# Kernel tuning notes

Measured on AMD Instinct MI355X. Metric: run time of the kernel, lower is better.

The kernel has to match this reference:

```python
import jax, jax.numpy as jnp
import numpy as np


def setup_inputs() -> dict:
    key = jax.random.key(0)
    ks = jax.random.split(key, 8)
    B, L, D = 4, 2048, 2048
    H, Dh, S = 24, 64, 64
    Di = H * Dh              # 1536
    P = H * (1 + 2 * S)      # 3096
    return {
        "hidden_states": jax.random.normal(ks[0], (B, L, D), jnp.float32),
        "norm_w": jnp.ones((D,), jnp.float32),
        "in_proj_w": jax.random.normal(ks[1], (2 * Di, D), jnp.float32) * 0.02,
        "in_proj_b": jnp.zeros((2 * Di,), jnp.float32),
        "conv_w": jax.random.normal(ks[2], (Di, 1, 4), jnp.float32) * 0.2,
        "conv_b": jnp.zeros((Di,), jnp.float32),
        "x_proj_w": jax.random.normal(ks[3], (P, Di), jnp.float32) * 0.02,
        "x_proj_b": jnp.zeros((P,), jnp.float32),
        "A_log": jnp.full((H,), np.log(0.5), jnp.float32),
        "log2_alpha_base": jnp.full((H,), -1.0, jnp.float32),
        "log2_beta": jnp.zeros((H,), jnp.float32),
        "surprise_ema": jnp.ones((H,), jnp.float32),
        "out_proj_w": jax.random.normal(ks[4], (D, Di), jnp.float32) * 0.02,
        "out_proj_b": jnp.zeros((D,), jnp.float32),
        "res_gate": jnp.full((1,), 1.0 / np.sqrt(2 * 24), jnp.float32),
    }


def reference(hidden_states, norm_w, in_proj_w, in_proj_b, conv_w, conv_b,
              x_proj_w, x_proj_b, A_log, log2_alpha_base, log2_beta,
              surprise_ema, out_proj_w, out_proj_b, res_gate):
    Bsz, L, D = hidden_states.shape
    H = A_log.shape[0]
    S = (x_proj_b.shape[0] // H - 1) // 2
    Di = in_proj_w.shape[0] // 2
    Dh = Di // H
    eps = jnp.finfo(jnp.float32).eps

    # RMSNorm
    x = hidden_states * jax.lax.rsqrt(jnp.mean(hidden_states ** 2, -1, keepdims=True) + eps) * norm_w
    # in_proj -> split x/z
    xz = x @ in_proj_w.T + in_proj_b
    x, z = xz[..., :Di], xz[..., Di:]
    # causal depthwise conv1d (kernel 4, left pad 3 == torch pad=3 then [:, :L])
    xc = jax.lax.conv_general_dilated(
        x.transpose(0, 2, 1), conv_w, (1,), [(3, 0)],
        dimension_numbers=("NCH", "OIH", "NCH"), feature_group_count=Di)
    x = jax.nn.silu((xc + conv_b[None, :, None]).transpose(0, 2, 1))
    # x_proj -> dt, B, C
    xp = (x @ x_proj_w.T + x_proj_b).reshape(Bsz, L, H, 1 + 2 * S)
    dt = xp[..., 0]
    Bs = xp[..., 1:1 + S]
    Cs = xp[..., 1 + S:]
    Bs = Bs / jnp.maximum(jnp.linalg.norm(Bs, axis=-1, keepdims=True), 1e-12)
    Cs = Cs / jnp.maximum(jnp.linalg.norm(Cs, axis=-1, keepdims=True), 1e-12)
    # dt-scaled log decay (dt_scale = softplus(dt))
    A = jnp.clip(A_log, -2.3, -0.01)[None, None, :] * jax.nn.softplus(dt)
    A_decay = jnp.exp(A)                       # [B, L, H]
    X = x.reshape(Bsz, L, H, Dh)

    # surprise-gate constants (eval mode: EMA buffer fixed)
    alpha_base = 1.0 - 2.0 ** jnp.clip(log2_alpha_base, -3.32, -0.015)   # [H]
    beta = 2.0 ** jnp.clip(log2_beta, -2.0, 2.0)                          # [H]

    def step(carry, xs):
        h, h_red = carry                      # [B,H,S,Dh], [B,H,S]
        x_t, a_t, B_t, C_t = xs               # [B,H,Dh], [B,H], [B,H,S], [B,H,S]
        u_red = B_t * x_t.mean(-1)[..., None]                 # mean over Dh of outer product
        diff = (1.0 - a_t)[..., None] * u_red                 # h_new_reduced - h_expected
        pe = jnp.mean(diff ** 2, -1)                          # [B,H]
        ns = pe / (surprise_ema[None, :] + 1e-6)
        boost = jax.nn.relu(jnp.tanh(beta[None, :] * ns))
        alpha = jnp.clip(alpha_base[None, :] + (1.0 - alpha_base[None, :]) * boost, 0.01, 0.999)
        u_t = B_t[..., None] * x_t[:, :, None, :]             # [B,H,S,Dh]
        h = alpha[..., None, None] * h + (1.0 - alpha)[..., None, None] * u_t
        h_red = h.mean(-1)
        y = jnp.einsum("bhs,bhsd->bhd", C_t, h)
        return (h, h_red), y

    h0 = jnp.zeros((Bsz, H, S, Dh), jnp.float32)
    hr0 = jnp.zeros((Bsz, H, S), jnp.float32)
    xs = (X.transpose(1, 0, 2, 3), A_decay.transpose(1, 0, 2),
          Bs.transpose(1, 0, 2, 3), Cs.transpose(1, 0, 2, 3))
    _, Yt = jax.lax.scan(step, (h0, hr0), xs)                 # [L,B,H,Dh]
    Y = Yt.transpose(1, 0, 2, 3).reshape(Bsz, L, Di)
    Y = Y * jax.nn.silu(z)
    out = Y @ out_proj_w.T + out_proj_b
    return hidden_states + res_gate * out
```

## Files before the change

### kernel.cpp

```cpp
#include <hip/hip_runtime.h>
#include <stdint.h>

#define BB 4
#define LLEN 2048
#define DMODEL 2048
#define NH 24
#define DH 64
#define SS 64
#define DI 1536
#define N2 3072
#define NP 3096
#define NP_PAD 3200
#define MROWS 8192
#define NCHUNK 16
#define QC 128

using bf16x8 = __bf16 __attribute__((ext_vector_type(8)));
using f32x4  = float __attribute__((ext_vector_type(4)));

__device__ __forceinline__ unsigned short f2bf(float f) {
  union { float f; unsigned int u; } v; v.f = f;
  unsigned int u = v.u + 0x7fffu + ((v.u >> 16) & 1u);
  return (unsigned short)(u >> 16);
}
__device__ __forceinline__ float bf2f(unsigned short h) {
  union { unsigned int u; float f; } v; v.u = ((unsigned int)h) << 16;
  return v.f;
}

__device__ __forceinline__ void gload16(const void* g, void* l) {
  __builtin_amdgcn_global_load_lds(
    reinterpret_cast<const __attribute__((address_space(1))) void*>(reinterpret_cast<uintptr_t>(g)),
    reinterpret_cast<__attribute__((address_space(3))) void*>((uint32_t)(reinterpret_cast<uintptr_t>(l))),
    16, 0, 0);
}

__global__ __launch_bounds__(256) void k_w2bf(const float* __restrict__ s,
                                              unsigned short* __restrict__ d,
                                              int n_src, int n_dst) {
  int i = blockIdx.x * 256 + threadIdx.x;
  if (i < n_dst) d[i] = (i < n_src) ? f2bf(s[i]) : (unsigned short)0;
}

__global__ __launch_bounds__(256) void k_rmsnorm(const float* __restrict__ hs,
                                                 const float* __restrict__ w,
                                                 unsigned short* __restrict__ out) {
  const int row = blockIdx.x;
  const int t = threadIdx.x;
  const float* x = hs + (size_t)row * DMODEL;
  float4 v0 = reinterpret_cast<const float4*>(x)[t * 2 + 0];
  float4 v1 = reinterpret_cast<const float4*>(x)[t * 2 + 1];
  float ss = v0.x * v0.x + v0.y * v0.y + v0.z * v0.z + v0.w * v0.w +
             v1.x * v1.x + v1.y * v1.y + v1.z * v1.z + v1.w * v1.w;
#pragma unroll
  for (int o = 32; o; o >>= 1) ss += __shfl_xor(ss, o);
  __shared__ float red[4];
  if ((t & 63) == 0) red[t >> 6] = ss;
  __syncthreads();
  ss = red[0] + red[1] + red[2] + red[3];
  const float r = rsqrtf(ss * (1.0f / DMODEL) + 1.1920928955078125e-07f);
  float4 w0 = reinterpret_cast<const float4*>(w)[t * 2 + 0];
  float4 w1 = reinterpret_cast<const float4*>(w)[t * 2 + 1];
  union { unsigned short u[8]; uint4 v; } pk;
  pk.u[0] = f2bf(v0.x * r * w0.x); pk.u[1] = f2bf(v0.y * r * w0.y);
  pk.u[2] = f2bf(v0.z * r * w0.z); pk.u[3] = f2bf(v0.w * r * w0.w);
  pk.u[4] = f2bf(v1.x * r * w1.x); pk.u[5] = f2bf(v1.y * r * w1.y);
  pk.u[6] = f2bf(v1.z * r * w1.z); pk.u[7] = f2bf(v1.w * r * w1.w);
  *reinterpret_cast<uint4*>(out + (size_t)row * DMODEL + t * 8) = pk.v;
}

template <int EPI, int BMH>
__global__ __launch_bounds__(512, 2)
void k_gemm5(const unsigned short* __restrict__ A, const unsigned short* __restrict__ B,
             const float* __restrict__ bias, void* __restrict__ Cv,
             const float* __restrict__ resid, const float* __restrict__ gatep,
             int K, int NT_N, int Nout, int ldc) {
  constexpr int NSET = BMH / 64;
  constexpr int AELEM = BMH * 64;
  constexpr int BUFE = AELEM + 16384;
  __shared__ alignas(16) unsigned short sm[2 * BUFE];
  const int tid = threadIdx.x;
  const int lane = tid & 63, wid = tid >> 6;
  const int wm = wid >> 2, wn = wid & 3;
  const int fr = lane & 15, kg = lane >> 4;
  const int nwg = gridDim.x;
  const int wg = ((int)blockIdx.x & 7) * (nwg >> 3) + ((int)blockIdx.x >> 3);
  const int m0 = (wg / NT_N) * BMH, n0 = (wg % NT_N) * 256;
  const int NT = K >> 6;

  const unsigned short* asrc[NSET];
  const unsigned short* bsrc[4];
#pragma unroll
  for (int li = 0; li < NSET; ++li) {
    const int gi = li * 512 + tid, r = gi >> 3, q = gi & 7;
    asrc[li] = A + (size_t)(m0 + r) * K + ((q ^ (r & 7)) << 3);
  }
#pragma unroll
  for (int li = 0; li < 4; ++li) {
    const int gi = li * 512 + tid, r = gi >> 3, q = gi & 7;
    bsrc[li] = B + (size_t)(n0 + r) * K + ((q ^ (r & 7)) << 3);
  }
  const int wlds = wid * 64;

#define STG5(buf, ko)                                                          \
  { unsigned short* da_ = sm + (buf) * BUFE;                                   \
    _Pragma("unroll") for (int li = 0; li < NSET; ++li)                        \
      gload16(asrc[li] + (ko), da_ + ((li * 512 + wlds) << 3));                \
    unsigned short* db_ = sm + (buf) * BUFE + AELEM;                           \
    _Pragma("unroll") for (int li = 0; li < 4; ++li)                           \
      gload16(bsrc[li] + (ko), db_ + ((li * 512 + wlds) << 3)); }

#define ARD5(bufp, f, kk)                                                      \
  (*(const bf16x8*)((bufp) +                                                   \
      (((f) < 4 ? wm * 64 + (f) * 16 : 128 + wm * 64 + ((f) - 4) * 16) + fr) * 64 + \
      ((((kk) * 4 + kg) ^ (fr & 7)) << 3)))
#define BRD5(bufp, nf, kk)                                                     \
  (*(const bf16x8*)((bufp) + AELEM + (wn * 64 + (nf) * 16 + fr) * 64 +         \
      ((((kk) * 4 + kg) ^ (fr & 7)) << 3)))

  f32x4 acc[2 * NSET][4] = {};

  STG5(0, 0)
  asm volatile("s_waitcnt vmcnt(0)" ::: "memory");
  __builtin_amdgcn_s_barrier();

  for (int t = 0; t < NT; ++t) {
    unsigned short* bc = sm + (t & 1) * BUFE;
    if (t + 1 < NT) STG5((t & 1) ^ 1, (t + 1) << 6)

    bf16x8 bfv[4][2], af[2][2][2];
#pragma unroll
    for (int nf = 0; nf < 4; ++nf) {
      bfv[nf][0] = BRD5(bc, nf, 0);
      bfv[nf][1] = BRD5(bc, nf, 1);
    }
#pragma unroll
    for (int s = 0; s < 2; ++s)
#pragma unroll
      for (int mf = 0; mf < 2; ++mf)
#pragma unroll
        for (int kk = 0; kk < 2; ++kk)
          af[s][mf][kk] = ARD5(bc, s * 2 + mf, kk);
    __builtin_amdgcn_sched_barrier(0);
    asm volatile("s_waitcnt lgkmcnt(0)" ::: "memory");
    __builtin_amdgcn_sched_barrier(0);
    __builtin_amdgcn_s_setprio(1);
#pragma unroll
    for (int s = 0; s < 2; ++s)
#pragma unroll
      for (int mf = 0; mf < 2; ++mf)
#pragma unroll
        for (int nf = 0; nf < 4; ++nf)
#pragma unroll
          for (int kk = 0; kk < 2; ++kk)
            acc[s * 2 + mf][nf] = __builtin_amdgcn_mfma_f32_16x16x32_bf16(
                af[s][mf][kk], bfv[nf][kk], acc[s * 2 + mf][nf], 0, 0, 0);
    __builtin_amdgcn_s_setprio(0);

    if (NSET == 4) {
      bf16x8 ag[2][2][2];
#pragma unroll
      for (int s = 0; s < 2; ++s)
#pragma unroll
        for (int mf = 0; mf < 2; ++mf)
#pragma unroll
          for (int kk = 0; kk < 2; ++kk)
            ag[s][mf][kk] = ARD5(bc, 4 + s * 2 + mf, kk);
      __builtin_amdgcn_sched_barrier(0);
      asm volatile("s_waitcnt lgkmcnt(0)" ::: "memory");
      __builtin_amdgcn_sched_barrier(0);
      __builtin_amdgcn_s_setprio(1);
#pragma unroll
      for (int s = 0; s < 2; ++s)
#pragma unroll
        for (int mf = 0; mf < 2; ++mf)
#pragma unroll
          for (int nf = 0; nf < 4; ++nf)
#pragma unroll
            for (int kk = 0; kk < 2; ++kk)
              acc[4 + s * 2 + mf][nf] = __builtin_amdgcn_mfma_f32_16x16x32_bf16(
                  ag[s][mf][kk], bfv[nf][kk], acc[4 + s * 2 + mf][nf], 0, 0, 0);
      __builtin_amdgcn_s_setprio(0);
    }

    asm volatile("s_waitcnt vmcnt(0)" ::: "memory");
    __builtin_amdgcn_s_barrier();
  }

  float* Cf = (float*)Cv;
  unsigned short* Ch = (unsigned short*)Cv;
  const float rg = (EPI == 2) ? gatep[0] : 0.f;
#pragma unroll
  for (int nf = 0; nf < 4; ++nf) {
    const int col = n0 + wn * 64 + nf * 16 + fr;
    if (col >= Nout) continue;
    const float bv = bias[col];
#pragma unroll
    for (int mf = 0; mf < 2 * NSET; ++mf) {
      const int rowb = m0 + ((mf < 4) ? wm * 64 + mf * 16
                                      : 128 + wm * 64 + (mf - 4) * 16) + kg * 4;
#pragma unroll
      for (int r = 0; r < 4; ++r) {
        const size_t o = (size_t)(rowb + r) * ldc + col;
        float v = acc[mf][nf][r] + bv;
        if (EPI == 1) {
          Ch[o] = f2bf(v);
        } else {
          if (EPI == 2) v = resid[o] + rg * v;
          Cf[o] = v;
        }
      }
    }
  }
#undef STG5
#undef ARD5
#undef BRD5
}

__global__ __launch_bounds__(256) void k_dwconv(const unsigned short* __restrict__ xz,
                                                const float* __restrict__ cw,
                                                const float* __restrict__ cb,
                                                unsigned short* __restrict__ out) {
  const int idx = blockIdx.x * 256 + threadIdx.x;
  const int c0 = (idx % 192) * 8;
  const int bl0 = (idx / 192) * 4;
  const int lpos0 = bl0 & (LLEN - 1);
  float w[8][4];
#pragma unroll
  for (int j = 0; j < 8; ++j) {
    const float4 wv = *(const float4*)(cw + (c0 + j) * 4);
    w[j][0] = wv.x; w[j][1] = wv.y; w[j][2] = wv.z; w[j][3] = wv.w;
  }
  float xr[7][8];
#pragma unroll
  for (int m = 0; m < 7; ++m) {
    uint4 xv = make_uint4(0u, 0u, 0u, 0u);
    if (lpos0 - 3 + m >= 0)
      xv = *(const uint4*)(xz + (size_t)(bl0 - 3 + m) * N2 + c0);
    const unsigned short* xs = (const unsigned short*)&xv;
#pragma unroll
    for (int j = 0; j < 8; ++j) xr[m][j] = bf2f(xs[j]);
  }
  const float4 cb0 = *(const float4*)(cb + c0);
  const float4 cb1 = *(const float4*)(cb + c0 + 4);
  const float cbv[8] = {cb0.x, cb0.y, cb0.z, cb0.w, cb1.x, cb1.y, cb1.z, cb1.w};
#pragma unroll
  for (int t4 = 0; t4 < 4; ++t4) {
    union { unsigned short u[8]; uint4 v; } pk;
#pragma unroll
    for (int j = 0; j < 8; ++j) {
      float a = cbv[j];
#pragma unroll
      for (int k = 0; k < 4; ++k) a = fmaf(w[j][k], xr[t4 + k][j], a);
      a = a / (1.f + __expf(-a));
      pk.u[j] = f2bf(a);
    }
    *(uint4*)(out + (size_t)(bl0 + t4) * DI + c0) = pk.v;
  }
}

__global__ __launch_bounds__(256) void k_prep(const unsigned short* __restrict__ xp,
                                              const unsigned short* __restrict__ xc,
                                              const float* __restrict__ A_log,
                                              const float* __restrict__ l2ab,
                                              const float* __restrict__ l2b,
                                              const float* __restrict__ se,
                                              unsigned short* __restrict__ Bn,
                                              unsigned short* __restrict__ Cn,
                                              float* __restrict__ al) {
  const int blk = blockIdx.x;
  const int w = threadIdx.x >> 6, lane = threadIdx.x & 63;
  const int bl = blk / 6, hq = blk % 6;
  const int h = hq * 4 + w;
  const size_t pbase = (size_t)bl * NP_PAD + h * 129;
  const float bs = bf2f(xp[pbase + 1 + lane]);
  const float cs = bf2f(xp[pbase + 65 + lane]);
  const float xv = bf2f(xc[(size_t)bl * DI + h * DH + lane]);
  float sb = bs * bs, sc = cs * cs, sx = xv;
#pragma unroll
  for (int o = 32; o; o >>= 1) {
    sb += __shfl_xor(sb, o);
    sc += __shfl_xor(sc, o);
    sx += __shfl_xor(sx, o);
  }
  const float nb = fmaxf(sqrtf(sb), 1e-12f);
  const float nc = fmaxf(sqrtf(sc), 1e-12f);
  const int b = bl >> 11, l = bl & (LLEN - 1);
  const size_t ob = (((size_t)(b * NH + h) << 11) + l) * 64 + lane;
  Bn[ob] = f2bf(bs / nb);
  Cn[ob] = f2bf(cs / nc);
  const float sumB2 = sb / (nb * nb);
  const float xmean = sx * (1.f / 64.f);
  const float dt = bf2f(xp[pbase]);
  const float sp = (dt > 20.f) ? dt : log1pf(expf(dt));
  const float Ac = fminf(fmaxf(A_log[h], -2.3f), -0.01f);
  const float aa = expf(Ac * sp);
  const float one_a = 1.f - aa;
  const float pe = one_a * one_a * xmean * xmean * sumB2 * (1.f / 64.f);
  const float ns = pe / (se[h] + 1e-6f);
  const float beta = exp2f(fminf(fmaxf(l2b[h], -2.f), 2.f));
  const float boost = fmaxf(tanhf(beta * ns), 0.f);
  const float ab = 1.f - exp2f(fminf(fmaxf(l2ab[h], -3.32f), -0.015f));
  const float alpha = fminf(fmaxf(ab + (1.f - ab) * boost, 0.01f), 0.999f);
  if (lane == 0) al[(((size_t)b * NH + h) << 11) + l] = alpha;
}

__global__ __launch_bounds__(256) void k_chunk1(
    const unsigned short* __restrict__ Bn, const unsigned short* __restrict__ Cn,
    const unsigned short* __restrict__ xcg, const float* __restrict__ al,
    unsigned short* __restrict__ xz, unsigned short* __restrict__ Hbuf,
    float* __restrict__ Dc) {
  const int blk = blockIdx.x;
  const int bh = blk >> 4, c = blk & 15;
  const int b = bh / NH, h = bh % NH;
  const int tid = threadIdx.x, w = tid >> 6, lane = tid & 63;
  const int fr = lane & 15, kg = lane >> 4;
  const int rbase = b * LLEN + c * QC;
  const size_t bcb = (((size_t)bh << 11) + c * QC) * 64;

  __shared__ float lc[QC], ia[QC], escl[QC];
  __shared__ float wtot[2];
  __shared__ alignas(16) unsigned short XT[64][152];
  __shared__ alignas(16) unsigned short BsT[64][152];
  __shared__ alignas(16) unsigned short Pt[128][88];

  float a = 1.f, la = 0.f;
  if (tid < QC) { a = al[(size_t)bh * LLEN + c * QC + tid]; la = __logf(a); }
  float s = la;
#pragma unroll
  for (int o = 1; o < 64; o <<= 1) { float t2 = __shfl_up(s, o); if (lane >= o) s += t2; }
  if (tid < QC && lane == 63) wtot[w] = s;
  __syncthreads();
  if (tid < QC) { lc[tid] = s + ((w == 1) ? wtot[0] : 0.f); ia[tid] = 1.f - a; }
  __syncthreads();
  const float lcE = lc[QC - 1];
  if (tid < QC) escl[tid] = __expf(lcE - lc[tid]) * ia[tid];
  if (tid == 0) Dc[blk] = __expf(lcE);
  __syncthreads();

  {
    const int r8 = tid >> 3, q8 = tid & 7;
#pragma unroll
    for (int it = 0; it < 4; ++it) {
      const int u = it * 32 + r8;
      const uint4 xv = *(const uint4*)(xcg + (size_t)(rbase + u) * DI + h * DH + q8 * 8);
      const unsigned short* xs = (const unsigned short*)&xv;
#pragma unroll
      for (int j = 0; j < 8; ++j) XT[q8 * 8 + j][u] = xs[j];
      const uint4 bv = *(const uint4*)(Bn + bcb + (size_t)u * 64 + q8 * 8);
      const unsigned short* bsv = (const unsigned short*)&bv;
      const float e = escl[u];
#pragma unroll
      for (int j = 0; j < 8; ++j) BsT[q8 * 8 + j][u] = f2bf(bf2f(bsv[j]) * e);
    }
  }
  bf16x8 cf[2][2];
#pragma unroll
  for (int fi = 0; fi < 2; ++fi)
#pragma unroll
    for (int kk = 0; kk < 2; ++kk) {
      const int t = w * 32 + fi * 16 + fr;
      const uint4 v = *(const uint4*)(Cn + bcb + (size_t)t * 64 + kk * 32 + kg * 8);
      cf[fi][kk] = *(const bf16x8*)&v;
    }
  __syncthreads();

  float lct[2][4];
#pragma unroll
  for (int fi = 0; fi < 2; ++fi)
#pragma unroll
    for (int r = 0; r < 4; ++r) lct[fi][r] = lc[w * 32 + fi * 16 + kg * 4 + r];

  f32x4 yacc[2][4] = {};
  f32x4 hacc[4] = {};
#pragma unroll
  for (int ut = 0; ut < 2; ++ut) {
    f32x4 g[2][4] = {};
#pragma unroll
    for (int kk = 0; kk < 2; ++kk)
#pragma unroll
      for (int fj = 0; fj < 4; ++fj) {
        const int u = ut * 64 + fj * 16 + fr;
        const uint4 v = *(const uint4*)(Bn + bcb + (size_t)u * 64 + kk * 32 + kg * 8);
        const bf16x8 bfrag = *(const bf16x8*)&v;
#pragma unroll
        for (int fi = 0; fi < 2; ++fi)
          g[fi][fj] = __builtin_amdgcn_mfma_f32_16x16x32_bf16(cf[fi][kk], bfrag, g[fi][fj], 0, 0, 0);
      }
#pragma unroll
    for (int fi = 0; fi < 2; ++fi)
#pragma unroll
      for (int fj = 0; fj < 4; ++fj) {
        const int u = ut * 64 + fj * 16 + fr;
        const float lcu = lc[u], iau = ia[u];
#pragma unroll
        for (int r = 0; r < 4; ++r) {
          const int t = w * 32 + fi * 16 + kg * 4 + r;
          const float v = (t >= u) ? g[fi][fj][r] * __expf(lct[fi][r] - lcu) * iau : 0.f;
          Pt[t][fj * 16 + fr] = f2bf(v);
        }
      }
#pragma unroll
    for (int kk = 0; kk < 2; ++kk) {
      bf16x8 xf[4];
#pragma unroll
      for (int fj = 0; fj < 4; ++fj)
        xf[fj] = *(const bf16x8*)&XT[fj * 16 + fr][ut * 64 + kk * 32 + kg * 8];
      bf16x8 pf[2];
#pragma unroll
      for (int fi = 0; fi < 2; ++fi)
        pf[fi] = *(const bf16x8*)&Pt[w * 32 + fi * 16 + fr][kk * 32 + kg * 8];
#pragma unroll
      for (int fi = 0; fi < 2; ++fi)
#pragma unroll
        for (int fj = 0; fj < 4; ++fj)
          yacc[fi][fj] = __builtin_amdgcn_mfma_f32_16x16x32_bf16(pf[fi], xf[fj], yacc[fi][fj], 0, 0, 0);
      const bf16x8 xh = *(const bf16x8*)&XT[w * 16 + fr][ut * 64 + kk * 32 + kg * 8];
#pragma unroll
      for (int fi = 0; fi < 4; ++fi) {
        const bf16x8 bs = *(const bf16x8*)&BsT[fi * 16 + fr][ut * 64 + kk * 32 + kg * 8];
        hacc[fi] = __builtin_amdgcn_mfma_f32_16x16x32_bf16(bs, xh, hacc[fi], 0, 0, 0);
      }
    }
  }
#pragma unroll
  for (int fi = 0; fi < 2; ++fi)
#pragma unroll
    for (int fj = 0; fj < 4; ++fj)
#pragma unroll
      for (int r = 0; r < 4; ++r) {
        const int t = w * 32 + fi * 16 + kg * 4 + r;
        const int d = fj * 16 + fr;
        xz[(size_t)(rbase + t) * N2 + h * DH + d] = f2bf(yacc[fi][fj][r]);
      }
  const int dcol = w * 16 + fr;
#pragma unroll
  for (int fi = 0; fi < 4; ++fi) {
    ushort4 pk;
    pk.x = f2bf(hacc[fi][0]); pk.y = f2bf(hacc[fi][1]);
    pk.z = f2bf(hacc[fi][2]); pk.w = f2bf(hacc[fi][3]);
    *(ushort4*)(Hbuf + ((size_t)blk * 64 + dcol) * 64 + fi * 16 + kg * 4) = pk;
  }
}

__global__ __launch_bounds__(256) void k_carry(unsigned short* __restrict__ Hbuf,
                                               const float* __restrict__ Dc) {
  const int bh = blockIdx.x, tid = threadIdx.x;
  float carry[16];
#pragma unroll
  for (int j = 0; j < 16; ++j) carry[j] = 0.f;
  for (int c = 0; c < NCHUNK; ++c) {
    unsigned short* p = Hbuf + (((size_t)(bh * NCHUNK + c)) << 12) + tid * 16;
    const uint4 v0 = *(const uint4*)(p);
    const uint4 v1 = *(const uint4*)(p + 8);
    const unsigned short* hs0 = (const unsigned short*)&v0;
    const unsigned short* hs1 = (const unsigned short*)&v1;
    float hl[16];
#pragma unroll
    for (int j = 0; j < 8; ++j) { hl[j] = bf2f(hs0[j]); hl[8 + j] = bf2f(hs1[j]); }
    uint4 o0, o1;
    unsigned short* os0 = (unsigned short*)&o0;
    unsigned short* os1 = (unsigned short*)&o1;
#pragma unroll
    for (int j = 0; j < 8; ++j) { os0[j] = f2bf(carry[j]); os1[j] = f2bf(carry[8 + j]); }
    *(uint4*)(p) = o0;
    *(uint4*)(p + 8) = o1;
    const float dc = Dc[bh * NCHUNK + c];
#pragma unroll
    for (int j = 0; j < 16; ++j) carry[j] = fmaf(dc, carry[j], hl[j]);
  }
}

__global__ __launch_bounds__(256) void k_chunk2(
    const unsigned short* __restrict__ Cn, const float* __restrict__ al,
    const unsigned short* __restrict__ Hbuf, const unsigned short* __restrict__ xz,
    unsigned short* __restrict__ xcg) {
  const int blk = blockIdx.x;
  const int bh = blk >> 4, c = blk & 15;
  const int b = bh / NH, h = bh % NH;
  const int tid = threadIdx.x, w = tid >> 6, lane = tid & 63;
  const int fr = lane & 15, kg = lane >> 4;
  const int rbase = b * LLEN + c * QC;
  const size_t bcb = (((size_t)bh << 11) + c * QC) * 64;
  __shared__ float lc[QC];
  __shared__ float wtot[2];
  float a = 1.f, la = 0.f;
  if (tid < QC) { a = al[(size_t)bh * LLEN + c * QC + tid]; la = __logf(a); }
  float s = la;
#pragma unroll
  for (int o = 1; o < 64; o <<= 1) { float t2 = __shfl_up(s, o); if (lane >= o) s += t2; }
  if (tid < QC && lane == 63) wtot[w] = s;
  __syncthreads();
  if (tid < QC) lc[tid] = s + ((w == 1) ? wtot[0] : 0.f);
  __syncthreads();
  bf16x8 cf[2][2];
#pragma unroll
  for (int fi = 0; fi < 2; ++fi) {
    const int t = w * 32 + fi * 16 + fr;
    const float sc = __expf(lc[t]);
#pragma unroll
    for (int kk = 0; kk < 2; ++kk) {
      const uint4 v = *(const uint4*)(Cn + bcb + (size_t)t * 64 + kk * 32 + kg * 8);
      const unsigned short* cs = (const unsigned short*)&v;
      union { unsigned short us[8]; bf16x8 vv; } uv;
#pragma unroll
      for (int q = 0; q < 8; ++q) uv.us[q] = f2bf(bf2f(cs[q]) * sc);
      cf[fi][kk] = uv.vv;
    }
  }
  bf16x8 hf[4][2];
#pragma unroll
  for (int fj = 0; fj < 4; ++fj)
#pragma unroll
    for (int kk = 0; kk < 2; ++kk) {
      const uint4 v = *(const uint4*)(Hbuf + ((size_t)blk * 64 + fj * 16 + fr) * 64 + kk * 32 + kg * 8);
      hf[fj][kk] = *(const bf16x8*)&v;
    }
  f32x4 y[2][4] = {};
#pragma unroll
  for (int kk = 0; kk < 2; ++kk)
#pragma unroll
    for (int fi = 0; fi < 2; ++fi)
#pragma unroll
      for (int fj = 0; fj < 4; ++fj)
        y[fi][fj] = __builtin_amdgcn_mfma_f32_16x16x32_bf16(cf[fi][kk], hf[fj][kk], y[fi][fj], 0, 0, 0);
#pragma unroll
  for (int fi = 0; fi < 2; ++fi)
#pragma unroll
    for (int fj = 0; fj < 4; ++fj)
#pragma unroll
      for (int r = 0; r < 4; ++r) {
        const int t = w * 32 + fi * 16 + kg * 4 + r;
        const int d = fj * 16 + fr;
        const size_t rowg = (size_t)(rbase + t);
        const float yv = y[fi][fj][r] + bf2f(xz[rowg * N2 + h * DH + d]);
        const float zv = bf2f(xz[rowg * N2 + DI + h * DH + d]);
        const float g = yv * (zv / (1.f + __expf(-zv)));
        xcg[rowg * DI + h * DH + d] = f2bf(g);
      }
}

extern "C" void kernel_launch(void* const* d_in, const int* in_sizes, int n_in,
                              void* d_out, int out_size, void* d_ws, size_t ws_size,
                              hipStream_t stream) {
  const float* hs     = (const float*)d_in[0];
  const float* norm_w = (const float*)d_in[1];
  const float* in_w   = (const float*)d_in[2];
  const float* in_b   = (const float*)d_in[3];
  const float* cw     = (const float*)d_in[4];
  const float* cb     = (const float*)d_in[5];
  const float* xw     = (const float*)d_in[6];
  const float* xb     = (const float*)d_in[7];
  const float* A_log  = (const float*)d_in[8];
  const float* l2ab   = (const float*)d_in[9];
  const float* l2b    = (const float*)d_in[10];
  const float* se     = (const float*)d_in[11];
  const float* ow     = (const float*)d_in[12];
  const float* ob     = (const float*)d_in[13];
  const float* rg     = (const float*)d_in[14];
  float* out = (float*)d_out;

  char* ws = (char*)d_ws;
  unsigned short* xnorm = (unsigned short*)(ws);
  unsigned short* wA    = (unsigned short*)(ws + 33554432ull);
  unsigned short* wX    = (unsigned short*)(ws + 46137344ull);
  unsigned short* wO    = (unsigned short*)(ws + 55967744ull);
  unsigned short* xz    = (unsigned short*)(ws + 62259200ull);
  unsigned short* xp    = (unsigned short*)(ws + 112590848ull);
  unsigned short* Bn    = (unsigned short*)(ws + 165019648ull);
  unsigned short* Cn    = (unsigned short*)(ws + 190185472ull);
  unsigned short* xcg   = xnorm;
  unsigned short* Hbuf  = wA;
  float* al             = (float*)(ws + 46137344ull);
  float* Dc             = (float*)(ws + 46137344ull + 786432ull);

  k_w2bf<<<(N2 * DMODEL) / 256, 256, 0, stream>>>(in_w, wA, N2 * DMODEL, N2 * DMODEL);
  k_w2bf<<<(NP_PAD * DI) / 256, 256, 0, stream>>>(xw, wX, NP * DI, NP_PAD * DI);
  k_w2bf<<<(DMODEL * DI) / 256, 256, 0, stream>>>(ow, wO, DMODEL * DI, DMODEL * DI);

  k_rmsnorm<<<MROWS, 256, 0, stream>>>(hs, norm_w, xnorm);
  k_gemm5<1, 128><<<768, 512, 0, stream>>>(xnorm, wA, in_b, xz, nullptr, nullptr,
                                           DMODEL, 12, N2, N2);
  k_dwconv<<<(MROWS / 4) * 192 / 256, 256, 0, stream>>>(xz, cw, cb, xcg);
  k_gemm5<1, 256><<<416, 512, 0, stream>>>(xcg, wX, xb, xp, nullptr, nullptr,
                                           DI, 13, NP, NP_PAD);
  k_prep<<<MROWS * 6, 256, 0, stream>>>(xp, xcg, A_log, l2ab, l2b, se, Bn, Cn, al);

  k_chunk1<<<BB * NH * NCHUNK, 256, 0, stream>>>(Bn, Cn, xcg, al, xz, Hbuf, Dc);
  k_carry<<<BB * NH, 256, 0, stream>>>(Hbuf, Dc);
  k_chunk2<<<BB * NH * NCHUNK, 256, 0, stream>>>(Cn, al, Hbuf, xz, xcg);

  k_gemm5<2, 256><<<256, 512, 0, stream>>>(xcg, wO, ob, out, hs, rg,
                                           DI, 8, DMODEL, DMODEL);
}
```

Measured before the change: 507.0 us.

## Switch GEMMs to triple-buffered LDS pipeline with uniform 128-row tiles

Replaces the double-buffered GEMM with a three-stage LDS ring that prefetches two K-tiles ahead and waits only for the older tile's loads (vmcnt(6)) rather than draining all loads each iteration. The 256-row tile variant is dropped, so all three GEMMs use 128x256 tiles and the x_proj and out_proj grids double. This aims to hide global-load latency better and raise workgroup count for the smaller GEMMs. In exchange it uses more shared memory per block, which may limit occupancy, and smaller tiles reload the B operand more often.

```diff
diff --git a/kernel.cpp b/kernel.cpp
--- a/kernel.cpp
+++ b/kernel.cpp
@@ -69,29 +69,28 @@
   *reinterpret_cast<uint4*>(out + (size_t)row * DMODEL + t * 8) = pk.v;
 }
 
-template <int EPI, int BMH>
+template <int EPI>
 __global__ __launch_bounds__(512, 2)
-void k_gemm5(const unsigned short* __restrict__ A, const unsigned short* __restrict__ B,
+void k_gemm6(const unsigned short* __restrict__ A, const unsigned short* __restrict__ B,
              const float* __restrict__ bias, void* __restrict__ Cv,
              const float* __restrict__ resid, const float* __restrict__ gatep,
              int K, int NT_N, int Nout, int ldc) {
-  constexpr int NSET = BMH / 64;
-  constexpr int AELEM = BMH * 64;
+  constexpr int AELEM = 128 * 64;
   constexpr int BUFE = AELEM + 16384;
-  __shared__ alignas(16) unsigned short sm[2 * BUFE];
+  __shared__ alignas(16) unsigned short sm[3 * BUFE];
   const int tid = threadIdx.x;
   const int lane = tid & 63, wid = tid >> 6;
   const int wm = wid >> 2, wn = wid & 3;
   const int fr = lane & 15, kg = lane >> 4;
   const int nwg = gridDim.x;
   const int wg = ((int)blockIdx.x & 7) * (nwg >> 3) + ((int)blockIdx.x >> 3);
-  const int m0 = (wg / NT_N) * BMH, n0 = (wg % NT_N) * 256;
+  const int m0 = (wg / NT_N) * 128, n0 = (wg % NT_N) * 256;
   const int NT = K >> 6;
 
-  const unsigned short* asrc[NSET];
+  const unsigned short* asrc[2];
   const unsigned short* bsrc[4];
 #pragma unroll
-  for (int li = 0; li < NSET; ++li) {
+  for (int li = 0; li < 2; ++li) {
     const int gi = li * 512 + tid, r = gi >> 3, q = gi & 7;
     asrc[li] = A + (size_t)(m0 + r) * K + ((q ^ (r & 7)) << 3);
   }
@@ -102,89 +101,64 @@
   }
   const int wlds = wid * 64;
 
-#define STG5(buf, ko)                                                          \
+#define STG6(buf, ko)                                                          \
   { unsigned short* da_ = sm + (buf) * BUFE;                                   \
-    _Pragma("unroll") for (int li = 0; li < NSET; ++li)                        \
-      gload16(asrc[li] + (ko), da_ + ((li * 512 + wlds) << 3));                \
+    gload16(asrc[0] + (ko), da_ + ((0 * 512 + wlds) << 3));                    \
+    gload16(asrc[1] + (ko), da_ + ((1 * 512 + wlds) << 3));                    \
     unsigned short* db_ = sm + (buf) * BUFE + AELEM;                           \
     _Pragma("unroll") for (int li = 0; li < 4; ++li)                           \
       gload16(bsrc[li] + (ko), db_ + ((li * 512 + wlds) << 3)); }
 
-#define ARD5(bufp, f, kk)                                                      \
-  (*(const bf16x8*)((bufp) +                                                   \
-      (((f) < 4 ? wm * 64 + (f) * 16 : 128 + wm * 64 + ((f) - 4) * 16) + fr) * 64 + \
+#define ARD6(bufp, f, kk)                                                      \
+  (*(const bf16x8*)((bufp) + (wm * 64 + (f) * 16 + fr) * 64 +                  \
       ((((kk) * 4 + kg) ^ (fr & 7)) << 3)))
-#define BRD5(bufp, nf, kk)                                                     \
+#define BRD6(bufp, nf, kk)                                                     \
   (*(const bf16x8*)((bufp) + AELEM + (wn * 64 + (nf) * 16 + fr) * 64 +         \
       ((((kk) * 4 + kg) ^ (fr & 7)) << 3)))
 
-  f32x4 acc[2 * NSET][4] = {};
-
-  STG5(0, 0)
-  asm volatile("s_waitcnt vmcnt(0)" ::: "memory");
+  f32x4 acc[4][4] = {};
+
+  STG6(0, 0)
+  STG6(1, 64)
+  asm volatile("s_waitcnt vmcnt(6)" ::: "memory");
   __builtin_amdgcn_s_barrier();
 
+  int bc_i = 0;
   for (int t = 0; t < NT; ++t) {
-    unsigned short* bc = sm + (t & 1) * BUFE;
-    if (t + 1 < NT) STG5((t & 1) ^ 1, (t + 1) << 6)
-
-    bf16x8 bfv[4][2], af[2][2][2];
+    unsigned short* bc = sm + bc_i * BUFE;
+    const int bn_i = (bc_i + 2 >= 3) ? (bc_i - 1) : (bc_i + 2);
+    const bool st = (t + 2) < NT;
+    if (st) STG6(bn_i, (t + 2) << 6)
+
+    bf16x8 bfv[4][2], af[4][2];
 #pragma unroll
     for (int nf = 0; nf < 4; ++nf) {
-      bfv[nf][0] = BRD5(bc, nf, 0);
-      bfv[nf][1] = BRD5(bc, nf, 1);
-    }
-#pragma unroll
-    for (int s = 0; s < 2; ++s)
-#pragma unroll
-      for (int mf = 0; mf < 2; ++mf)
-#pragma unroll
-        for (int kk = 0; kk < 2; ++kk)
-          af[s][mf][kk] = ARD5(bc, s * 2 + mf, kk);
+      bfv[nf][0] = BRD6(bc, nf, 0);
+      bfv[nf][1] = BRD6(bc, nf, 1);
+    }
+#pragma unroll
+    for (int mf = 0; mf < 4; ++mf) {
+      af[mf][0] = ARD6(bc, mf, 0);
+      af[mf][1] = ARD6(bc, mf, 1);
+    }
     __builtin_amdgcn_sched_barrier(0);
     asm volatile("s_waitcnt lgkmcnt(0)" ::: "memory");
     __builtin_amdgcn_sched_barrier(0);
     __builtin_amdgcn_s_setprio(1);
 #pragma unroll
-    for (int s = 0; s < 2; ++s)
-#pragma unroll
-      for (int mf = 0; mf < 2; ++mf)
-#pragma unroll
-        for (int nf = 0; nf < 4; ++nf)
-#pragma unroll
-          for (int kk = 0; kk < 2; ++kk)
-            acc[s * 2 + mf][nf] = __builtin_amdgcn_mfma_f32_16x16x32_bf16(
-                af[s][mf][kk], bfv[nf][kk], acc[s * 2 + mf][nf], 0, 0, 0);
+    for (int mf = 0; mf < 4; ++mf)
+#pragma unroll
+      for (int nf = 0; nf < 4; ++nf)
+#pragma unroll
+        for (int kk = 0; kk < 2; ++kk)
+          acc[mf][nf] = __builtin_amdgcn_mfma_f32_16x16x32_bf16(
+              af[mf][kk], bfv[nf][kk], acc[mf][nf], 0, 0, 0);
     __builtin_amdgcn_s_setprio(0);
 
-    if (NSET == 4) {
-      bf16x8 ag[2][2][2];
-#pragma unroll
-      for (int s = 0; s < 2; ++s)
-#pragma unroll
-        for (int mf = 0; mf < 2; ++mf)
-#pragma unroll
-          for (int kk = 0; kk < 2; ++kk)
-            ag[s][mf][kk] = ARD5(bc, 4 + s * 2 + mf, kk);
-      __builtin_amdgcn_sched_barrier(0);
-      asm volatile("s_waitcnt lgkmcnt(0)" ::: "memory");
-      __builtin_amdgcn_sched_barrier(0);
-      __builtin_amdgcn_s_setprio(1);
-#pragma unroll
-      for (int s = 0; s < 2; ++s)
-#pragma unroll
-        for (int mf = 0; mf < 2; ++mf)
-#pragma unroll
-          for (int nf = 0; nf < 4; ++nf)
-#pragma unroll
-            for (int kk = 0; kk < 2; ++kk)
-              acc[4 + s * 2 + mf][nf] = __builtin_amdgcn_mfma_f32_16x16x32_bf16(
-                  ag[s][mf][kk], bfv[nf][kk], acc[4 + s * 2 + mf][nf], 0, 0, 0);
-      __builtin_amdgcn_s_setprio(0);
-    }
-
-    asm volatile("s_waitcnt vmcnt(0)" ::: "memory");
+    if (st) { asm volatile("s_waitcnt vmcnt(6)" ::: "memory"); }
+    else    { asm volatile("s_waitcnt vmcnt(0)" ::: "memory"); }
     __builtin_amdgcn_s_barrier();
+    bc_i = (bc_i + 1 >= 3) ? 0 : (bc_i + 1);
   }
 
   float* Cf = (float*)Cv;
@@ -196,9 +170,8 @@
     if (col >= Nout) continue;
     const float bv = bias[col];
 #pragma unroll
-    for (int mf = 0; mf < 2 * NSET; ++mf) {
-      const int rowb = m0 + ((mf < 4) ? wm * 64 + mf * 16
-                                      : 128 + wm * 64 + (mf - 4) * 16) + kg * 4;
+    for (int mf = 0; mf < 4; ++mf) {
+      const int rowb = m0 + wm * 64 + mf * 16 + kg * 4;
 #pragma unroll
       for (int r = 0; r < 4; ++r) {
         const size_t o = (size_t)(rowb + r) * ldc + col;
@@ -212,9 +185,9 @@
       }
     }
   }
-#undef STG5
-#undef ARD5
-#undef BRD5
+#undef STG6
+#undef ARD6
+#undef BRD6
 }
 
 __global__ __launch_bounds__(256) void k_dwconv(const unsigned short* __restrict__ xz,
@@ -579,17 +552,17 @@
   k_w2bf<<<(DMODEL * DI) / 256, 256, 0, stream>>>(ow, wO, DMODEL * DI, DMODEL * DI);
 
   k_rmsnorm<<<MROWS, 256, 0, stream>>>(hs, norm_w, xnorm);
-  k_gemm5<1, 128><<<768, 512, 0, stream>>>(xnorm, wA, in_b, xz, nullptr, nullptr,
-                                           DMODEL, 12, N2, N2);
+  k_gemm6<1><<<768, 512, 0, stream>>>(xnorm, wA, in_b, xz, nullptr, nullptr,
+                                      DMODEL, 12, N2, N2);
   k_dwconv<<<(MROWS / 4) * 192 / 256, 256, 0, stream>>>(xz, cw, cb, xcg);
-  k_gemm5<1, 256><<<416, 512, 0, stream>>>(xcg, wX, xb, xp, nullptr, nullptr,
-                                           DI, 13, NP, NP_PAD);
+  k_gemm6<1><<<832, 512, 0, stream>>>(xcg, wX, xb, xp, nullptr, nullptr,
+                                      DI, 13, NP, NP_PAD);
   k_prep<<<MROWS * 6, 256, 0, stream>>>(xp, xcg, A_log, l2ab, l2b, se, Bn, Cn, al);
 
   k_chunk1<<<BB * NH * NCHUNK, 256, 0, stream>>>(Bn, Cn, xcg, al, xz, Hbuf, Dc);
   k_carry<<<BB * NH, 256, 0, stream>>>(Hbuf, Dc);
   k_chunk2<<<BB * NH * NCHUNK, 256, 0, stream>>>(Cn, al, Hbuf, xz, xcg);
 
-  k_gemm5<2, 256><<<256, 512, 0, stream>>>(xcg, wO, ob, out, hs, rg,
-                                           DI, 8, DMODEL, DMODEL);
-}
+  k_gemm6<2><<<512, 512, 0, stream>>>(xcg, wO, ob, out, hs, rg,
+                                      DI, 8, DMODEL, DMODEL);
+}
```

New measurement: 531.5 us. +4.8%, slower.
